# Optimization experiments

Measured on AMD Instinct MI355X. Metric: run time of the kernel, lower is better.

## Reference

```python
import jax, jax.numpy as jnp
import numpy as np

NUM_GROUPS = 8
ROUTING_ITERS = 3
EPS = 1e-8

def setup_inputs() -> dict:
    key = jax.random.key(0)
    ks = jax.random.split(key, 6)
    B, C, H, W = 16, 256, 64, 64
    Cq = C // 4
    G = NUM_GROUPS
    x = jax.random.normal(ks[0], (B, C, H, W), jnp.float32)
    group_assignments = jax.random.uniform(ks[1], (B, C, G), jnp.float32)
    conv_w = jax.random.normal(ks[2], (Cq, C), jnp.float32) * 0.05
    conv_b = jax.random.normal(ks[3], (Cq,), jnp.float32) * 0.05
    lin_w = jax.random.normal(ks[4], (C * G, Cq), jnp.float32) * 0.05
    lin_b = jax.random.normal(ks[5], (C * G,), jnp.float32) * 0.05
    return {"x": x, "group_assignments": group_assignments,
            "conv_w": conv_w, "conv_b": conv_b, "lin_w": lin_w, "lin_b": lin_b}

def reference(x, group_assignments, conv_w, conv_b, lin_w, lin_b):
    B, C, H, W = x.shape
    G = NUM_GROUPS
    # routing_predictor: 1x1 conv (pure channel mix) -> ReLU -> global avg pool -> linear
    h = jax.nn.relu(jnp.einsum('bchw,dc->bdhw', x, conv_w) + conv_b[None, :, None, None])
    pooled = h.mean(axis=(2, 3))                               # (B, C//4)
    logits = (pooled @ lin_w.T + lin_b).reshape(B, C, G)       # (B, C, G)
    logits = logits + jnp.log(group_assignments + EPS)
    xf = x.reshape(B, C, H * W)                                # (B, C, N)
    x_norm = jnp.maximum(jnp.linalg.norm(xf, axis=2), EPS)     # (B, C)
    # dynamic routing: last iteration's softmax/group-sum contributes nothing to output,
    # so only ROUTING_ITERS-1 agreement updates are applied (same math as torch code)
    for _ in range(ROUTING_ITERS - 1):
        w = jax.nn.softmax(logits, axis=-1)                    # (B, C, G)
        s = jnp.einsum('bcg,bcn->bgn', w, xf)                  # group outputs (B, G, N)
        s_norm = jnp.maximum(jnp.linalg.norm(s, axis=2), EPS)  # (B, G)
        sim = jnp.einsum('bcn,bgn->bcg', xf, s) / (x_norm[:, :, None] * s_norm[:, None, :])
        logits = logits + sim
    final_weights = jax.nn.softmax(logits, axis=-1)
    return final_weights, x
```

## Files before the change

### kernel.cpp

```cpp
#include <hip/hip_runtime.h>

#define BB 16
#define CC 256
#define NN 4096
#define CN (CC*NN)
#define GG 8
#define EPSF 1e-8f
#define NT 64

typedef __attribute__((ext_vector_type(8))) short bf16x8;
typedef __attribute__((ext_vector_type(4))) float f32x4;
typedef __attribute__((ext_vector_type(2))) unsigned int uint32x2;

__device__ __forceinline__ unsigned short bfr(float f) {
  unsigned int u = __float_as_uint(f);
  return (unsigned short)((u + 0x7FFFu + ((u >> 16) & 1u)) >> 16);
}

__global__ __launch_bounds__(512, 4) void k_prep(const float* __restrict__ x,
                                                 const float* __restrict__ conv_w,
                                                 const float* __restrict__ conv_b,
                                                 float* __restrict__ xout,
                                                 float* __restrict__ xnp,
                                                 float* __restrict__ pooledpart,
                                                 unsigned short* __restrict__ xbf_g) {
  const int b = blockIdx.x >> 6;
  const int chunk = blockIdx.x & 63;
  const int t = threadIdx.x;
  const int lane = t & 63, wv = t >> 6;
  __shared__ unsigned short xbf[16384];
  __shared__ float pool[8 * 16];

  const int dt = wv >> 1, h2 = wv & 1;
  const int g = lane >> 4, col = lane & 15;
  const int drow = dt * 16 + col;
  union AF { uint4 q; bf16x8 v; unsigned short u[8]; } a[8];
  {
    const float* wrow = conv_w + (size_t)drow * 256;
#pragma unroll
    for (int kk = 0; kk < 8; ++kk) {
      float4 w0 = *(const float4*)(wrow + kk * 32 + g * 8);
      float4 w1 = *(const float4*)(wrow + kk * 32 + g * 8 + 4);
      a[kk].u[0] = bfr(w0.x); a[kk].u[1] = bfr(w0.y);
      a[kk].u[2] = bfr(w0.z); a[kk].u[3] = bfr(w0.w);
      a[kk].u[4] = bfr(w1.x); a[kk].u[5] = bfr(w1.y);
      a[kk].u[6] = bfr(w1.z); a[kk].u[7] = bfr(w1.w);
    }
  }

  const float* xb = x + (size_t)b * CN + chunk * NT;
  const int r0 = t >> 4, j = t & 15;
  float4 v[8];
  float sq[8];
#pragma unroll
  for (int k = 0; k < 8; ++k)
    v[k] = *(const float4*)(xb + (size_t)(k * 32 + r0) * NN + j * 4);
#pragma unroll
  for (int k = 0; k < 8; ++k) {
    ushort4 hh;
    hh.x = bfr(v[k].x); hh.y = bfr(v[k].y); hh.z = bfr(v[k].z); hh.w = bfr(v[k].w);
    *(ushort4*)&xbf[(k * 4 + (j >> 2)) * 512 + r0 * 16 + (j & 3) * 4] = hh;
    sq[k] = v[k].x * v[k].x + v[k].y * v[k].y + v[k].z * v[k].z + v[k].w * v[k].w;
  }
  float* xo = xout + (size_t)b * CN + chunk * NT;
#pragma unroll
  for (int k = 0; k < 8; ++k)
    *(float4*)(xo + (size_t)(k * 32 + r0) * NN + j * 4) = v[k];
#pragma unroll
  for (int k = 0; k < 8; ++k) {
    float s = sq[k];
    s += __shfl_xor(s, 1, 64); s += __shfl_xor(s, 2, 64);
    s += __shfl_xor(s, 4, 64); s += __shfl_xor(s, 8, 64);
    sq[k] = s;
  }
  if ((t & 15) == 0) {
    float* xp = xnp + ((size_t)b * 64 + chunk) * 256 + r0;
#pragma unroll
    for (int k = 0; k < 8; ++k) xp[k * 32] = sq[k];
  }
  __syncthreads();

  {
    uint4* xgo4 = (uint4*)(xbf_g + (size_t)(b * 64 + chunk) * 16384);
    const uint4* xl4 = (const uint4*)xbf;
#pragma unroll
    for (int k = 0; k < 4; ++k) xgo4[k * 512 + t] = xl4[k * 512 + t];
  }

  f32x4 acc0 = {0.f, 0.f, 0.f, 0.f}, acc1 = {0.f, 0.f, 0.f, 0.f};
  const unsigned int xbase = (unsigned int)(size_t)&xbf[0];
  const unsigned int lanoff = (unsigned int)(col * 2 + g * 256);
#pragma unroll
  for (int kk = 0; kk < 8; ++kk) {
    const unsigned int ra = xbase + (unsigned int)((kk * 4 + 2 * h2) * 1024) + lanoff;
    const unsigned int rb = ra + 1024;
    union BF { uint32x2 tr[2]; bf16x8 v; } b0, b1;
    asm volatile("ds_read_b64_tr_b16 %0, %1" : "=v"(b0.tr[0]) : "v"(ra));
    asm volatile("ds_read_b64_tr_b16 %0, %1" : "=v"(b0.tr[1]) : "v"(ra + 128));
    asm volatile("ds_read_b64_tr_b16 %0, %1" : "=v"(b1.tr[0]) : "v"(rb));
    asm volatile("ds_read_b64_tr_b16 %0, %1" : "=v"(b1.tr[1]) : "v"(rb + 128));
    asm volatile("s_waitcnt lgkmcnt(0)" ::: "memory");
    __builtin_amdgcn_sched_barrier(0);
    acc0 = __builtin_amdgcn_mfma_f32_16x16x32_bf16(a[kk].v, b0.v, acc0, 0, 0, 0);
    acc1 = __builtin_amdgcn_mfma_f32_16x16x32_bf16(a[kk].v, b1.v, acc1, 0, 0, 0);
  }
  const float4 bias = *(const float4*)(conv_b + dt * 16 + 4 * g);
  const float br[4] = {bias.x, bias.y, bias.z, bias.w};
  float hs[4];
#pragma unroll
  for (int r = 0; r < 4; ++r) {
    float hv = fmaxf(acc0[r] + br[r], 0.f) + fmaxf(acc1[r] + br[r], 0.f);
    hv += __shfl_xor(hv, 1, 64); hv += __shfl_xor(hv, 2, 64);
    hv += __shfl_xor(hv, 4, 64); hv += __shfl_xor(hv, 8, 64);
    hs[r] = hv;
  }
  if (col == 0) {
#pragma unroll
    for (int r = 0; r < 4; ++r) pool[wv * 16 + g * 4 + r] = hs[r];
  }
  __syncthreads();
  if (t < 64) {
    const int dtt = t >> 4, idx = t & 15;
    pooledpart[((size_t)b * 64 + chunk) * 64 + t] =
        pool[(dtt * 2) * 16 + idx] + pool[(dtt * 2 + 1) * 16 + idx];
  }
}

__global__ __launch_bounds__(256) void k_logits(const float* __restrict__ pooledpart,
                                                const float* __restrict__ lin_w,
                                                const float* __restrict__ lin_b,
                                                const float* __restrict__ ga,
                                                float* __restrict__ logits,
                                                unsigned short* __restrict__ wgT) {
  const int b = blockIdx.x, t = threadIdx.x;
  __shared__ float ps2[4][64];
  __shared__ float ps[64];
  {
    const int d = t & 63, q = t >> 6;
    float s = 0.f;
#pragma unroll
    for (int k = 0; k < 16; ++k)
      s += pooledpart[((size_t)b * 64 + q * 16 + k) * 64 + d];
    ps2[q][d] = s;
  }
  __syncthreads();
  if (t < 64) ps[t] = (ps2[0][t] + ps2[1][t] + ps2[2][t] + ps2[3][t]) * (1.f / 4096.f);
  __syncthreads();
  const int c = t;
  float out[8];
#pragma unroll
  for (int g = 0; g < 8; ++g) {
    const float4* wr = (const float4*)(lin_w + ((size_t)c * 8 + g) * 64);
    float s = 0.f;
#pragma unroll
    for (int k4 = 0; k4 < 16; ++k4) {
      float4 wv = wr[k4];
      s += wv.x * ps[k4 * 4] + wv.y * ps[k4 * 4 + 1] + wv.z * ps[k4 * 4 + 2] +
           wv.w * ps[k4 * 4 + 3];
    }
    out[g] = s + lin_b[c * 8 + g] + logf(ga[((size_t)b * 256 + c) * 8 + g] + EPSF);
  }
  float* lp = logits + ((size_t)b * 256 + c) * 8;
  *(float4*)lp = make_float4(out[0], out[1], out[2], out[3]);
  *(float4*)(lp + 4) = make_float4(out[4], out[5], out[6], out[7]);
  float m = out[0];
#pragma unroll
  for (int g = 1; g < 8; ++g) m = fmaxf(m, out[g]);
  float sum = 0.f;
#pragma unroll
  for (int g = 0; g < 8; ++g) { out[g] = __expf(out[g] - m); sum += out[g]; }
  float r = 1.f / sum;
  unsigned short* wb = wgT + (size_t)b * 4096;
#pragma unroll
  for (int g = 0; g < 8; ++g) wb[g * 256 + c] = bfr(out[g] * r);
#pragma unroll
  for (int g = 8; g < 16; ++g) wb[g * 256 + c] = 0;
}

__global__ __launch_bounds__(512) void k_route(const unsigned short* __restrict__ xbf_g,
                                               const unsigned short* __restrict__ wgT,
                                               float* __restrict__ spart2,
                                               float* __restrict__ simpart) {
  const int b = blockIdx.x >> 6;
  const int chunk = blockIdx.x & 63;
  const int t = threadIdx.x;
  const int lane = t & 63, wv = t >> 6;
  const int col = lane & 15, grp = lane >> 4;
  __shared__ unsigned short xbf[16384];
  __shared__ unsigned short stb[1024];
  __shared__ float spool[64];

  {
    const uint4* xg = (const uint4*)(xbf_g + (size_t)(b * 64 + chunk) * 16384);
    uint4* xl = (uint4*)xbf;
#pragma unroll
    for (int k = 0; k < 4; ++k) xl[k * 512 + t] = xg[k * 512 + t];
  }
  __syncthreads();

  const unsigned int xbase = (unsigned int)(size_t)&xbf[0];
  const unsigned int sbase = (unsigned int)(size_t)&stb[0];
  const unsigned int lanoff = (unsigned int)(col * 2 + grp * 256);

  if (wv < 4) {
    const int nt = wv;
    union AF { uint4 q; bf16x8 v; } a[8];
    const uint4* wq = (const uint4*)(wgT + (size_t)b * 4096);
#pragma unroll
    for (int kk = 0; kk < 8; ++kk) a[kk].q = wq[col * 32 + kk * 4 + grp];
    f32x4 acc = {0.f, 0.f, 0.f, 0.f};
#pragma unroll
    for (int kk = 0; kk < 8; ++kk) {
      const unsigned int ra = xbase + (unsigned int)((kk * 4 + nt) * 1024) + lanoff;
      union BF { uint32x2 tr[2]; bf16x8 v; } bf;
      asm volatile("ds_read_b64_tr_b16 %0, %1" : "=v"(bf.tr[0]) : "v"(ra));
      asm volatile("ds_read_b64_tr_b16 %0, %1" : "=v"(bf.tr[1]) : "v"(ra + 128));
      asm volatile("s_waitcnt lgkmcnt(0)" ::: "memory");
      __builtin_amdgcn_sched_barrier(0);
      acc = __builtin_amdgcn_mfma_f32_16x16x32_bf16(a[kk].v, bf.v, acc, 0, 0, 0);
    }
    {
      ushort4 sv4;
      sv4.x = bfr(acc[0]); sv4.y = bfr(acc[1]); sv4.z = bfr(acc[2]); sv4.w = bfr(acc[3]);
      *(ushort4*)&stb[(nt >> 1) * 512 + ((nt & 1) * 16 + col) * 16 + 4 * grp] = sv4;
      float s2[4];
#pragma unroll
      for (int r = 0; r < 4; ++r) {
        float vv = acc[r] * acc[r];
        vv += __shfl_xor(vv, 1, 64); vv += __shfl_xor(vv, 2, 64);
        vv += __shfl_xor(vv, 4, 64); vv += __shfl_xor(vv, 8, 64);
        s2[r] = vv;
      }
      if (col == 0) {
#pragma unroll
        for (int r = 0; r < 4; ++r) spool[nt * 16 + 4 * grp + r] = s2[r];
      }
    }
  }
  __syncthreads();
  if (t < 8)
    spart2[((size_t)b * 64 + chunk) * 8 + t] =
        spool[t] + spool[16 + t] + spool[32 + t] + spool[48 + t];

  float* sp = simpart + ((size_t)b * 64 + chunk) * 2048;
#pragma unroll
  for (int m2 = 0; m2 < 2; ++m2) {
    const int mc = wv * 2 + m2;
    const int kkA = mc >> 1;
    const int rowin = (mc & 1) * 16 + col;
    f32x4 acc = {0.f, 0.f, 0.f, 0.f};
#pragma unroll
    for (int kh = 0; kh < 2; ++kh) {
      union AF { uint4 q; bf16x8 v; } aa;
      aa.q = *(const uint4*)&xbf[(kkA * 4 + kh * 2 + (grp >> 1)) * 512 + rowin * 16 +
                                 (grp & 1) * 8];
      const unsigned int rb = sbase + (unsigned int)(kh * 1024) + lanoff;
      union BF { uint32x2 tr[2]; bf16x8 v; } bs;
      asm volatile("ds_read_b64_tr_b16 %0, %1" : "=v"(bs.tr[0]) : "v"(rb));
      asm volatile("ds_read_b64_tr_b16 %0, %1" : "=v"(bs.tr[1]) : "v"(rb + 128));
      asm volatile("s_waitcnt lgkmcnt(0)" ::: "memory");
      __builtin_amdgcn_sched_barrier(0);
      acc = __builtin_amdgcn_mfma_f32_16x16x32_bf16(aa.v, bs.v, acc, 0, 0, 0);
    }
    if (col < 8) {
#pragma unroll
      for (int r = 0; r < 4; ++r)
        sp[(size_t)(mc * 16 + 4 * grp + r) * 8 + col] = acc[r];
    }
  }
}

template <int FINAL>
__global__ __launch_bounds__(256) void k_upd(const float* __restrict__ simpart,
                                             const float* __restrict__ xnp,
                                             const float* __restrict__ spart2,
                                             float* __restrict__ logits,
                                             float* __restrict__ xnorm,
                                             unsigned short* __restrict__ wgT,
                                             float* __restrict__ outw) {
  const int b = blockIdx.x >> 4;
  const int c0 = (blockIdx.x & 15) * 16;
  const int t = threadIdx.x;
  __shared__ float simld[16][8];
  __shared__ float xnl[16];
  __shared__ float snr8[8];
  {
    const int pair = t >> 1, kh = t & 1;
    const int cl = pair >> 3, g = pair & 7;
    float sm = 0.f;
    const float* sp = simpart + (((size_t)b * 64 + kh * 32) * 256 + c0 + cl) * 8 + g;
#pragma unroll 8
    for (int k = 0; k < 32; ++k) sm += sp[(size_t)k * 2048];
    sm += __shfl_xor(sm, 1, 64);
    if (kh == 0) simld[cl][g] = sm;
  }
  {
    const int cl2 = t >> 4, kq = t & 15;
    if (!FINAL) {
      float p = 0.f;
#pragma unroll
      for (int jj = 0; jj < 4; ++jj)
        p += xnp[((size_t)b * 64 + kq + 16 * jj) * 256 + c0 + cl2];
      p += __shfl_xor(p, 1, 64); p += __shfl_xor(p, 2, 64);
      p += __shfl_xor(p, 4, 64); p += __shfl_xor(p, 8, 64);
      if (kq == 0) {
        float xn = fmaxf(sqrtf(p), EPSF);
        xnl[cl2] = xn;
        xnorm[b * 256 + c0 + cl2] = xn;
      }
    } else {
      if (kq == 0) xnl[cl2] = xnorm[b * 256 + c0 + cl2];
    }
  }
  if (t < 64) {
    const int g2 = t >> 3, kq = t & 7;
    float p = 0.f;
#pragma unroll
    for (int jj = 0; jj < 8; ++jj) p += spart2[((size_t)b * 64 + kq + 8 * jj) * 8 + g2];
    p += __shfl_xor(p, 1, 64); p += __shfl_xor(p, 2, 64); p += __shfl_xor(p, 4, 64);
    if (kq == 0) snr8[g2] = 1.f / fmaxf(sqrtf(p), EPSF);
  }
  __syncthreads();
  if (t < 16) {
    const int c = c0 + t;
    float* lp = logits + ((size_t)b * 256 + c) * 8;
    float4 l0 = *(const float4*)lp, l1 = *(const float4*)(lp + 4);
    float lg[8] = {l0.x, l0.y, l0.z, l0.w, l1.x, l1.y, l1.z, l1.w};
    const float xni = 1.f / xnl[t];
#pragma unroll
    for (int g = 0; g < 8; ++g) lg[g] += simld[t][g] * xni * snr8[g];
    if (!FINAL) {
      *(float4*)lp = make_float4(lg[0], lg[1], lg[2], lg[3]);
      *(float4*)(lp + 4) = make_float4(lg[4], lg[5], lg[6], lg[7]);
    }
    float m = lg[0];
#pragma unroll
    for (int g = 1; g < 8; ++g) m = fmaxf(m, lg[g]);
    float sum = 0.f;
#pragma unroll
    for (int g = 0; g < 8; ++g) { lg[g] = __expf(lg[g] - m); sum += lg[g]; }
    float r = 1.f / sum;
    if (!FINAL) {
      unsigned short* wb = wgT + (size_t)b * 4096;
#pragma unroll
      for (int g = 0; g < 8; ++g) wb[g * 256 + c] = bfr(lg[g] * r);
#pragma unroll
      for (int g = 8; g < 16; ++g) wb[g * 256 + c] = 0;
    } else {
      float4* op = (float4*)(outw + ((size_t)b * 256 + c) * 8);
      op[0] = make_float4(lg[0] * r, lg[1] * r, lg[2] * r, lg[3] * r);
      op[1] = make_float4(lg[4] * r, lg[5] * r, lg[6] * r, lg[7] * r);
    }
  }
}

extern "C" void kernel_launch(void* const* d_in, const int* in_sizes, int n_in,
                              void* d_out, int out_size, void* d_ws, size_t ws_size,
                              hipStream_t stream) {
  const float* x = (const float*)d_in[0];
  const float* ga = (const float*)d_in[1];
  const float* conv_w = (const float*)d_in[2];
  const float* conv_b = (const float*)d_in[3];
  const float* lin_w = (const float*)d_in[4];
  const float* lin_b = (const float*)d_in[5];
  float* out = (float*)d_out;
  float* outx = out + 32768;

  float* ws = (float*)d_ws;
  float* pooledpart = ws;
  float* logits = ws + 81920;
  unsigned short* wgT = (unsigned short*)(ws + 114688);
  float* xnorm = ws + 147456;
  float* xnp = ws + 151552;
  float* spart2 = ws + 413696;
  float* simpart = ws + 421888;
  unsigned short* xbf_g = (unsigned short*)(ws + 2519040);

  k_prep<<<1024, 512, 0, stream>>>(x, conv_w, conv_b, outx, xnp, pooledpart, xbf_g);
  k_logits<<<16, 256, 0, stream>>>(pooledpart, lin_w, lin_b, ga, logits, wgT);

  k_route<<<1024, 512, 0, stream>>>(xbf_g, wgT, spart2, simpart);
  k_upd<0><<<256, 256, 0, stream>>>(simpart, xnp, spart2, logits, xnorm, wgT, out);

  k_route<<<1024, 512, 0, stream>>>(xbf_g, wgT, spart2, simpart);
  k_upd<1><<<256, 256, 0, stream>>>(simpart, xnp, spart2, logits, xnorm, wgT, out);
}
```

Before: 89.51 us.

## Split prep kernel into streaming copy/convert kernel and separate conv kernel

The fused prep kernel is split in two. A lightweight streaming kernel (2048 blocks of 256 threads, smaller LDS) copies x to the output with nontemporal stores, writes the bf16 tiles and computes the per-row squared norms. A separate conv kernel then reloads the bf16 tiles from global memory and runs the MFMA 1x1 conv and pooling. The aim is higher occupancy and better memory streaming in the bandwidth-bound copy, with the MFMA weights no longer competing for registers. The cost is an extra launch and an extra global read of the bf16 tiles.

```diff
diff --git a/kernel.cpp b/kernel.cpp
--- a/kernel.cpp
+++ b/kernel.cpp
@@ -17,13 +17,65 @@
   return (unsigned short)((u + 0x7FFFu + ((u >> 16) & 1u)) >> 16);
 }
 
-__global__ __launch_bounds__(512, 4) void k_prep(const float* __restrict__ x,
+__global__ __launch_bounds__(256) void k_stream(const float* __restrict__ x,
+                                                float* __restrict__ xout,
+                                                float* __restrict__ xnp,
+                                                unsigned short* __restrict__ xbf_g) {
+  const int blk = blockIdx.x;
+  const int b = blk >> 7;
+  const int chunk = (blk >> 1) & 63;
+  const int half = blk & 1;
+  const int t = threadIdx.x;
+  const int r0 = t >> 4, j = t & 15;
+  __shared__ unsigned short xs[8192];
+
+  const float* xb = x + (size_t)b * CN + chunk * NT;
+  float* xo = xout + (size_t)b * CN + chunk * NT;
+  float4 v[8];
+  float sq[8];
+#pragma unroll
+  for (int k = 0; k < 8; ++k)
+    v[k] = *(const float4*)(xb + (size_t)(half * 128 + k * 16 + r0) * NN + j * 4);
+#pragma unroll
+  for (int k = 0; k < 8; ++k) {
+    const int r = k * 16 + r0;
+    ushort4 hh;
+    hh.x = bfr(v[k].x); hh.y = bfr(v[k].y); hh.z = bfr(v[k].z); hh.w = bfr(v[k].w);
+    *(ushort4*)&xs[((r >> 5) * 4 + (j >> 2)) * 512 + (r & 31) * 16 + (j & 3) * 4] = hh;
+    sq[k] = v[k].x * v[k].x + v[k].y * v[k].y + v[k].z * v[k].z + v[k].w * v[k].w;
+  }
+#pragma unroll
+  for (int k = 0; k < 8; ++k) {
+    f32x4 nv;
+    nv.x = v[k].x; nv.y = v[k].y; nv.z = v[k].z; nv.w = v[k].w;
+    __builtin_nontemporal_store(
+        nv, (f32x4*)(xo + (size_t)(half * 128 + k * 16 + r0) * NN + j * 4));
+  }
+#pragma unroll
+  for (int k = 0; k < 8; ++k) {
+    float s = sq[k];
+    s += __shfl_xor(s, 1, 64); s += __shfl_xor(s, 2, 64);
+    s += __shfl_xor(s, 4, 64); s += __shfl_xor(s, 8, 64);
+    sq[k] = s;
+  }
+  if ((t & 15) == 0) {
+    float* xp = xnp + ((size_t)b * 64 + chunk) * 256 + half * 128 + r0;
+#pragma unroll
+    for (int k = 0; k < 8; ++k) xp[k * 16] = sq[k];
+  }
+  __syncthreads();
+  {
+    uint4* xgo4 = (uint4*)xbf_g + (size_t)(b * 64 + chunk) * 2048 + half * 1024;
+    const uint4* xl4 = (const uint4*)xs;
+#pragma unroll
+    for (int k = 0; k < 4; ++k) xgo4[k * 256 + t] = xl4[k * 256 + t];
+  }
+}
+
+__global__ __launch_bounds__(512, 4) void k_conv(const unsigned short* __restrict__ xbf_g,
                                                  const float* __restrict__ conv_w,
                                                  const float* __restrict__ conv_b,
-                                                 float* __restrict__ xout,
-                                                 float* __restrict__ xnp,
-                                                 float* __restrict__ pooledpart,
-                                                 unsigned short* __restrict__ xbf_g) {
+                                                 float* __restrict__ pooledpart) {
   const int b = blockIdx.x >> 6;
   const int chunk = blockIdx.x & 63;
   const int t = threadIdx.x;
@@ -47,45 +99,13 @@
       a[kk].u[6] = bfr(w1.z); a[kk].u[7] = bfr(w1.w);
     }
   }
-
-  const float* xb = x + (size_t)b * CN + chunk * NT;
-  const int r0 = t >> 4, j = t & 15;
-  float4 v[8];
-  float sq[8];
-#pragma unroll
-  for (int k = 0; k < 8; ++k)
-    v[k] = *(const float4*)(xb + (size_t)(k * 32 + r0) * NN + j * 4);
-#pragma unroll
-  for (int k = 0; k < 8; ++k) {
-    ushort4 hh;
-    hh.x = bfr(v[k].x); hh.y = bfr(v[k].y); hh.z = bfr(v[k].z); hh.w = bfr(v[k].w);
-    *(ushort4*)&xbf[(k * 4 + (j >> 2)) * 512 + r0 * 16 + (j & 3) * 4] = hh;
-    sq[k] = v[k].x * v[k].x + v[k].y * v[k].y + v[k].z * v[k].z + v[k].w * v[k].w;
-  }
-  float* xo = xout + (size_t)b * CN + chunk * NT;
-#pragma unroll
-  for (int k = 0; k < 8; ++k)
-    *(float4*)(xo + (size_t)(k * 32 + r0) * NN + j * 4) = v[k];
-#pragma unroll
-  for (int k = 0; k < 8; ++k) {
-    float s = sq[k];
-    s += __shfl_xor(s, 1, 64); s += __shfl_xor(s, 2, 64);
-    s += __shfl_xor(s, 4, 64); s += __shfl_xor(s, 8, 64);
-    sq[k] = s;
-  }
-  if ((t & 15) == 0) {
-    float* xp = xnp + ((size_t)b * 64 + chunk) * 256 + r0;
-#pragma unroll
-    for (int k = 0; k < 8; ++k) xp[k * 32] = sq[k];
-  }
-  __syncthreads();
-
-  {
-    uint4* xgo4 = (uint4*)(xbf_g + (size_t)(b * 64 + chunk) * 16384);
-    const uint4* xl4 = (const uint4*)xbf;
-#pragma unroll
-    for (int k = 0; k < 4; ++k) xgo4[k * 512 + t] = xl4[k * 512 + t];
-  }
+  {
+    const uint4* xg = (const uint4*)xbf_g + (size_t)(b * 64 + chunk) * 2048;
+    uint4* xl = (uint4*)xbf;
+#pragma unroll
+    for (int k = 0; k < 4; ++k) xl[k * 512 + t] = xg[k * 512 + t];
+  }
+  __syncthreads();
 
   f32x4 acc0 = {0.f, 0.f, 0.f, 0.f}, acc1 = {0.f, 0.f, 0.f, 0.f};
   const unsigned int xbase = (unsigned int)(size_t)&xbf[0];
@@ -191,7 +211,7 @@
   __shared__ float spool[64];
 
   {
-    const uint4* xg = (const uint4*)(xbf_g + (size_t)(b * 64 + chunk) * 16384);
+    const uint4* xg = (const uint4*)xbf_g + (size_t)(b * 64 + chunk) * 2048;
     uint4* xl = (uint4*)xbf;
 #pragma unroll
     for (int k = 0; k < 4; ++k) xl[k * 512 + t] = xg[k * 512 + t];
@@ -376,7 +396,8 @@
   float* simpart = ws + 421888;
   unsigned short* xbf_g = (unsigned short*)(ws + 2519040);
 
-  k_prep<<<1024, 512, 0, stream>>>(x, conv_w, conv_b, outx, xnp, pooledpart, xbf_g);
+  k_stream<<<2048, 256, 0, stream>>>(x, outx, xnp, xbf_g);
+  k_conv<<<1024, 512, 0, stream>>>(xbf_g, conv_w, conv_b, pooledpart);
   k_logits<<<16, 256, 0, stream>>>(pooledpart, lin_w, lin_b, ga, logits, wgT);
 
   k_route<<<1024, 512, 0, stream>>>(xbf_g, wgT, spart2, simpart);
```

Result: slower. 99.97 us (+11.7%).

## Split prep into contiguous streaming copy kernel and separate bf16 conv kernel

Applied to the files above, without the earlier changes.

The old fused prep kernel read x with strided 64-column chunks per channel. It is now split into k_stream and k_conv. k_stream reads long contiguous rows of x, writes the x copy with nontemporal stores, emits bf16 tiles and per-segment squared norms, and stores xbf_g in a new layout. k_conv and k_route reload their tiles from that layout, and k_upd reads the new xnp layout. The aim is better DRAM streaming efficiency for the large copy, at the cost of an extra launch and an extra bf16 read pass.

```diff
diff --git a/kernel.cpp b/kernel.cpp
--- a/kernel.cpp
+++ b/kernel.cpp
@@ -6,7 +6,6 @@
 #define CN (CC*NN)
 #define GG 8
 #define EPSF 1e-8f
-#define NT 64
 
 typedef __attribute__((ext_vector_type(8))) short bf16x8;
 typedef __attribute__((ext_vector_type(4))) float f32x4;
@@ -17,13 +16,64 @@
   return (unsigned short)((u + 0x7FFFu + ((u >> 16) & 1u)) >> 16);
 }
 
-__global__ __launch_bounds__(512, 4) void k_prep(const float* __restrict__ x,
+__global__ __launch_bounds__(256, 4) void k_stream(const float* __restrict__ x,
+                                                   float* __restrict__ xout,
+                                                   float* __restrict__ xnp,
+                                                   unsigned short* __restrict__ xbf_g) {
+  const int bid = blockIdx.x;
+  const int b = bid >> 6, cb = (bid >> 3) & 7, ns = bid & 7;
+  const int t = threadIdx.x, l = t & 63, w = t >> 6;
+  __shared__ unsigned short xs[16384];
+  const int c0 = cb * 32 + w * 8;
+  const int reg0 = l >> 2;
+  const int colo = (l & 3) * 4;
+  float sq[8];
+#pragma unroll
+  for (int rr = 0; rr < 8; ++rr) {
+    const int c = c0 + rr;
+    const float* src = x + (size_t)b * CN + (size_t)c * NN + ns * 512;
+    float* dst = xout + (size_t)b * CN + (size_t)c * NN + ns * 512;
+    float4 v0 = *(const float4*)(src + 4 * l);
+    float4 v1 = *(const float4*)(src + 256 + 4 * l);
+    f32x4 n0, n1;
+    n0.x = v0.x; n0.y = v0.y; n0.z = v0.z; n0.w = v0.w;
+    n1.x = v1.x; n1.y = v1.y; n1.z = v1.z; n1.w = v1.w;
+    __builtin_nontemporal_store(n0, (f32x4*)(dst + 4 * l));
+    __builtin_nontemporal_store(n1, (f32x4*)(dst + 256 + 4 * l));
+    const int crow = (w * 8 + rr) * 16;
+    ushort4 h0, h1;
+    h0.x = bfr(v0.x); h0.y = bfr(v0.y); h0.z = bfr(v0.z); h0.w = bfr(v0.w);
+    h1.x = bfr(v1.x); h1.y = bfr(v1.y); h1.z = bfr(v1.z); h1.w = bfr(v1.w);
+    *(ushort4*)&xs[(0 * 16 + reg0) * 512 + crow + colo] = h0;
+    *(ushort4*)&xs[(1 * 16 + reg0) * 512 + crow + colo] = h1;
+    sq[rr] = v0.x * v0.x + v0.y * v0.y + v0.z * v0.z + v0.w * v0.w +
+             v1.x * v1.x + v1.y * v1.y + v1.z * v1.z + v1.w * v1.w;
+  }
+#pragma unroll
+  for (int rr = 0; rr < 8; ++rr) {
+    float s = sq[rr];
+#pragma unroll
+    for (int off = 1; off < 64; off <<= 1) s += __shfl_xor(s, off, 64);
+    sq[rr] = s;
+  }
+  if (l == 0) {
+    float* xp = xnp + ((size_t)b * 256 + c0) * 8 + ns;
+#pragma unroll
+    for (int rr = 0; rr < 8; ++rr) xp[rr * 8] = sq[rr];
+  }
+  __syncthreads();
+  {
+    uint4* dst = (uint4*)xbf_g + (size_t)(b * 8 + cb) * 16384 + ns * 2048;
+    const uint4* xl4 = (const uint4*)xs;
+#pragma unroll
+    for (int k = 0; k < 8; ++k) dst[k * 256 + t] = xl4[k * 256 + t];
+  }
+}
+
+__global__ __launch_bounds__(512, 4) void k_conv(const unsigned short* __restrict__ xbf_g,
                                                  const float* __restrict__ conv_w,
                                                  const float* __restrict__ conv_b,
-                                                 float* __restrict__ xout,
-                                                 float* __restrict__ xnp,
-                                                 float* __restrict__ pooledpart,
-                                                 unsigned short* __restrict__ xbf_g) {
+                                                 float* __restrict__ pooledpart) {
   const int b = blockIdx.x >> 6;
   const int chunk = blockIdx.x & 63;
   const int t = threadIdx.x;
@@ -47,45 +97,17 @@
       a[kk].u[6] = bfr(w1.z); a[kk].u[7] = bfr(w1.w);
     }
   }
-
-  const float* xb = x + (size_t)b * CN + chunk * NT;
-  const int r0 = t >> 4, j = t & 15;
-  float4 v[8];
-  float sq[8];
-#pragma unroll
-  for (int k = 0; k < 8; ++k)
-    v[k] = *(const float4*)(xb + (size_t)(k * 32 + r0) * NN + j * 4);
-#pragma unroll
-  for (int k = 0; k < 8; ++k) {
-    ushort4 hh;
-    hh.x = bfr(v[k].x); hh.y = bfr(v[k].y); hh.z = bfr(v[k].z); hh.w = bfr(v[k].w);
-    *(ushort4*)&xbf[(k * 4 + (j >> 2)) * 512 + r0 * 16 + (j & 3) * 4] = hh;
-    sq[k] = v[k].x * v[k].x + v[k].y * v[k].y + v[k].z * v[k].z + v[k].w * v[k].w;
-  }
-  float* xo = xout + (size_t)b * CN + chunk * NT;
-#pragma unroll
-  for (int k = 0; k < 8; ++k)
-    *(float4*)(xo + (size_t)(k * 32 + r0) * NN + j * 4) = v[k];
-#pragma unroll
-  for (int k = 0; k < 8; ++k) {
-    float s = sq[k];
-    s += __shfl_xor(s, 1, 64); s += __shfl_xor(s, 2, 64);
-    s += __shfl_xor(s, 4, 64); s += __shfl_xor(s, 8, 64);
-    sq[k] = s;
-  }
-  if ((t & 15) == 0) {
-    float* xp = xnp + ((size_t)b * 64 + chunk) * 256 + r0;
-#pragma unroll
-    for (int k = 0; k < 8; ++k) xp[k * 32] = sq[k];
-  }
-  __syncthreads();
-
-  {
-    uint4* xgo4 = (uint4*)(xbf_g + (size_t)(b * 64 + chunk) * 16384);
-    const uint4* xl4 = (const uint4*)xbf;
-#pragma unroll
-    for (int k = 0; k < 4; ++k) xgo4[k * 512 + t] = xl4[k * 512 + t];
-  }
+  {
+    const int kk = t >> 6, q0 = t & 63;
+    const uint4* xg = (const uint4*)xbf_g + (size_t)(b * 8 + kk) * 16384 + chunk * 256;
+    uint4* xl = (uint4*)xbf;
+#pragma unroll
+    for (int jq = 0; jq < 4; ++jq) {
+      int q = jq * 64 + q0;
+      xl[kk * 256 + q] = xg[q];
+    }
+  }
+  __syncthreads();
 
   f32x4 acc0 = {0.f, 0.f, 0.f, 0.f}, acc1 = {0.f, 0.f, 0.f, 0.f};
   const unsigned int xbase = (unsigned int)(size_t)&xbf[0];
@@ -191,10 +213,14 @@
   __shared__ float spool[64];
 
   {
-    const uint4* xg = (const uint4*)(xbf_g + (size_t)(b * 64 + chunk) * 16384);
+    const int kk = t >> 6, q0 = t & 63;
+    const uint4* xg = (const uint4*)xbf_g + (size_t)(b * 8 + kk) * 16384 + chunk * 256;
     uint4* xl = (uint4*)xbf;
 #pragma unroll
-    for (int k = 0; k < 4; ++k) xl[k * 512 + t] = xg[k * 512 + t];
+    for (int jq = 0; jq < 4; ++jq) {
+      int q = jq * 64 + q0;
+      xl[kk * 256 + q] = xg[q];
+    }
   }
   __syncthreads();
 
@@ -297,10 +323,7 @@
   {
     const int cl2 = t >> 4, kq = t & 15;
     if (!FINAL) {
-      float p = 0.f;
-#pragma unroll
-      for (int jj = 0; jj < 4; ++jj)
-        p += xnp[((size_t)b * 64 + kq + 16 * jj) * 256 + c0 + cl2];
+      float p = (kq < 8) ? xnp[((size_t)b * 256 + c0 + cl2) * 8 + kq] : 0.f;
       p += __shfl_xor(p, 1, 64); p += __shfl_xor(p, 2, 64);
       p += __shfl_xor(p, 4, 64); p += __shfl_xor(p, 8, 64);
       if (kq == 0) {
@@ -376,7 +399,8 @@
   float* simpart = ws + 421888;
   unsigned short* xbf_g = (unsigned short*)(ws + 2519040);
 
-  k_prep<<<1024, 512, 0, stream>>>(x, conv_w, conv_b, outx, xnp, pooledpart, xbf_g);
+  k_stream<<<1024, 256, 0, stream>>>(x, outx, xnp, xbf_g);
+  k_conv<<<1024, 512, 0, stream>>>(xbf_g, conv_w, conv_b, pooledpart);
   k_logits<<<16, 256, 0, stream>>>(pooledpart, lin_w, lin_b, ga, logits, wgT);
 
   k_route<<<1024, 512, 0, stream>>>(xbf_g, wgT, spart2, simpart);
```

Result: slower. 100.3 us (+12.1%).
